# Kernel optimization log

Measured on AMD Instinct MI355X. Metric: run time of the kernel, lower is better.

## Reference

```python
import jax, jax.numpy as jnp
import numpy as np

S = 7          # grid
BBOX = 2       # boxes per cell
C = 20         # classes
IOU_T = 0.5
SCORE_T = 0.05
ORIG_H, ORIG_W = 448.0, 448.0
N = S * S * BBOX  # 98 candidate boxes per image


def _pairwise_iou(b):
    # b: [N,4] xyxy -> [N,N] IoU
    area = jnp.maximum(b[:, 2] - b[:, 0], 0.0) * jnp.maximum(b[:, 3] - b[:, 1], 0.0)
    x1 = jnp.maximum(b[:, None, 0], b[None, :, 0])
    y1 = jnp.maximum(b[:, None, 1], b[None, :, 1])
    x2 = jnp.minimum(b[:, None, 2], b[None, :, 2])
    y2 = jnp.minimum(b[:, None, 3], b[None, :, 3])
    inter = jnp.maximum(x2 - x1, 0.0) * jnp.maximum(y2 - y1, 0.0)
    union = area[:, None] + area[None, :] - inter
    return inter / jnp.maximum(union, 1e-9)


def _nms_keep(boxes, scores):
    # Greedy NMS (same math as torchvision.nms), then score threshold,
    # as in the original (threshold applied AFTER nms). Returns bool keep
    # mask in the ORIGINAL box order.
    order = jnp.argsort(-scores)
    M = _pairwise_iou(boxes[order])
    idx = jnp.arange(N)

    def body(i, keep):
        sup = (M[i] > IOU_T) & (idx > i) & keep[i]
        return keep & ~sup

    keep = jax.lax.fori_loop(0, N, body, jnp.ones(N, dtype=bool))
    keep = keep & (scores[order] >= SCORE_T)
    return jnp.zeros(N, dtype=bool).at[order].set(keep)


def _forward(x):
    B = x.shape[0]
    pred_cls = x[..., :C]                                   # [B,S,S,C]
    off = x[..., C:C + 4 * BBOX].reshape(B, S, S, BBOX, 4)  # [B,S,S,Bbox,4]
    conf = x[..., C + 4 * BBOX:C + 5 * BBOX]                # [B,S,S,Bbox]

    # YOLOv1 decode: cell-relative xy -> normalized image coords; wh already normalized.
    gy, gx = jnp.meshgrid(jnp.arange(S, dtype=x.dtype), jnp.arange(S, dtype=x.dtype), indexing="ij")
    cx = (off[..., 0] + gx[None, :, :, None]) / S
    cy = (off[..., 1] + gy[None, :, :, None]) / S
    w, h = off[..., 2], off[..., 3]
    boxes = jnp.stack([cx - w / 2, cy - h / 2, cx + w / 2, cy + h / 2], axis=-1)
    boxes = jnp.clip(boxes, 0.0, 1.0)
    scale = jnp.array([ORIG_W, ORIG_H, ORIG_W, ORIG_H], dtype=x.dtype)
    boxes_px = (boxes * scale).reshape(B, N, 4)             # [B,N,4] pixel xyxy

    cls_prob = jax.nn.softmax(pred_cls, axis=-1)            # [B,S,S,C]
    scores = (cls_prob[..., None, :] * conf[..., None]).reshape(B, N, C)  # [B,N,C]

    # Per-batch, per-class NMS, fully vectorized (boxes shared across classes).
    keep = jax.vmap(lambda bb, ss: jax.vmap(lambda s: _nms_keep(bb, s))(ss.T))(boxes_px, scores)  # [B,C,N]
    keep = keep.transpose(0, 2, 1).reshape(B, N * C)        # original (S,S,Bbox,C) flatten order

    cls_ids = jnp.tile(jnp.arange(C, dtype=x.dtype), N)     # [N*C]
    boxes_rep = jnp.repeat(boxes_px, C, axis=1)             # [B,N*C,4]
    out = jnp.concatenate([
        jnp.broadcast_to(cls_ids[None, :, None], (B, N * C, 1)),
        boxes_rep,
        scores.reshape(B, N * C, 1),
    ], axis=-1)                                             # [B,N*C,6] = [class,x1,y1,x2,y2,score]
    # Fixed-shape equivalent of the ragged torch output: suppressed rows zeroed.
    return out * keep[..., None].astype(x.dtype)


def setup_inputs() -> dict:
    key = jax.random.key(0)
    return {"inputs_ts": jax.random.normal(key, (1024, S, S, C + 5 * BBOX), dtype=jnp.float32)}


def reference(inputs_ts):
    return _forward(inputs_ts)
```

## Files before the change

### kernel.cpp

```cpp
#include <hip/hip_runtime.h>


namespace {
constexpr int kS    = 7;
constexpr int kC    = 20;
constexpr int kFeat = 30;
constexpr int kN    = 98;
constexpr int kRows = kN * kC;
constexpr int kOutF = kRows * 6;
constexpr int kT    = 256;
constexpr float kIouT   = 0.5f;
constexpr float kScoreT = 0.05f;
}

__device__ __forceinline__ float iou_f(float ax1, float ay1, float ax2, float ay2,
                                       float bx1, float by1, float bx2, float by2) {
#pragma clang fp contract(off)
    float aa = fmaxf(ax2 - ax1, 0.f) * fmaxf(ay2 - ay1, 0.f);
    float ab = fmaxf(bx2 - bx1, 0.f) * fmaxf(by2 - by1, 0.f);
    float ix1 = fmaxf(ax1, bx1);
    float iy1 = fmaxf(ay1, by1);
    float ix2 = fminf(ax2, bx2);
    float iy2 = fminf(ay2, by2);
    float inter = fmaxf(ix2 - ix1, 0.f) * fmaxf(iy2 - iy1, 0.f);
    float uni = aa + ab - inter;
    return inter / fmaxf(uni, 1e-9f);
}

__device__ __forceinline__ unsigned long long shfl64(unsigned long long v, int src) {
    unsigned lo = (unsigned)__shfl((int)(unsigned)(v & 0xffffffffull), src);
    unsigned hi = (unsigned)__shfl((int)(unsigned)(v >> 32), src);
    return ((unsigned long long)hi << 32) | lo;
}

__global__ __launch_bounds__(kT, 4) void yolo_head_kernel(const float* __restrict__ x,
                                                          float* __restrict__ out) {
    __shared__ float xs[kS * kS * kFeat];
    __shared__ float scT[kRows];
    __shared__ float maxp[kS * kS];
    __shared__ float x1s[kN], y1s[kN], x2s[kN], y2s[kN];
    __shared__ unsigned long long adjLo[kN], adjHi[kN];
    __shared__ float csc[4][kN];
    __shared__ unsigned short cid[4][kN];
    __shared__ unsigned short rnk[4][64];
    __shared__ unsigned short rid[4][64];
    __shared__ unsigned km[kC][4];

    const int b   = blockIdx.x;
    const int tid = threadIdx.x;
    const float* xb = x + (size_t)b * (kS * kS * kFeat);

    for (int e = tid; e < (kS * kS * kFeat) / 2; e += kT)
        reinterpret_cast<float2*>(xs)[e] = reinterpret_cast<const float2*>(xb)[e];
    __syncthreads();

    if (tid < kS * kS) {
#pragma clang fp contract(off)
        const int cell = tid;
        const float* p = &xs[cell * kFeat];
        float mx = p[0];
        for (int c = 1; c < kC; ++c) mx = fmaxf(mx, p[c]);
        float e[kC];
        float sum = 0.f;
        for (int c = 0; c < kC; ++c) { e[c] = expf(p[c] - mx); sum += e[c]; }
        const float conf0 = p[28], conf1 = p[29];
        for (int c = 0; c < kC; ++c) {
            float pr = e[c] / sum;
            scT[c * kN + 2 * cell]     = pr * conf0;
            scT[c * kN + 2 * cell + 1] = pr * conf1;
        }
        maxp[cell] = 1.0f / sum;
    } else if (tid >= 64 && tid < 64 + kN) {
#pragma clang fp contract(off)
        const int n = tid - 64;
        const int cell = n >> 1, k = n & 1;
        const int gi = cell / kS, gj = cell % kS;
        const float* p = &xs[cell * kFeat + kC + 4 * k];
        float cx = (p[0] + (float)gj) / 7.0f;
        float cy = (p[1] + (float)gi) / 7.0f;
        float w = p[2], h = p[3];
        x1s[n] = fminf(fmaxf(cx - w * 0.5f, 0.f), 1.f) * 448.f;
        y1s[n] = fminf(fmaxf(cy - h * 0.5f, 0.f), 1.f) * 448.f;
        x2s[n] = fminf(fmaxf(cx + w * 0.5f, 0.f), 1.f) * 448.f;
        y2s[n] = fminf(fmaxf(cy + h * 0.5f, 0.f), 1.f) * 448.f;
    }
    __syncthreads();

    const int wv   = tid >> 6;
    const int lane = tid & 63;
    const int nB   = (lane < kN - 64) ? lane + 64 : 0;

    {
        const float aX1 = x1s[lane], aY1 = y1s[lane], aX2 = x2s[lane], aY2 = y2s[lane];
        const float bX1 = x1s[nB],  bY1 = y1s[nB],  bX2 = x2s[nB],  bY2 = y2s[nB];
        const int cA = lane >> 1, kA = lane & 1;
        const bool uA = xs[cA * kFeat + 28 + kA] * maxp[cA] >= kScoreT;
        bool uB = false;
        if (lane < kN - 64) {
            const int cB = nB >> 1, kB = nB & 1;
            uB = xs[cB * kFeat + 28 + kB] * maxp[cB] >= kScoreT;
        }
        const unsigned long long ULo = __ballot(uA);
        const unsigned long long UHi = __ballot(uB);
        for (int i = wv; i < kN; i += 4) {
            const bool inU = (i < 64) ? ((ULo >> i) & 1ull) : ((UHi >> (i - 64)) & 1ull);
            if (!inU) continue;
            const float iX1 = x1s[i], iY1 = y1s[i], iX2 = x2s[i], iY2 = y2s[i];
            const bool oA = iou_f(iX1, iY1, iX2, iY2, aX1, aY1, aX2, aY2) > kIouT;
            const bool oB = (lane < kN - 64) &&
                            iou_f(iX1, iY1, iX2, iY2, bX1, bY1, bX2, bY2) > kIouT;
            const unsigned long long rLo = __ballot(oA);
            const unsigned long long rHi = __ballot(oB);
            if (lane == 0) { adjLo[i] = rLo; adjHi[i] = rHi; }
        }
    }
    __syncthreads();

    {
        const unsigned long long rowLoA = adjLo[lane], rowHiA = adjHi[lane];
        const unsigned long long rowLoB = adjLo[nB],   rowHiB = adjHi[nB];
        const unsigned long long selfA  = 1ull << lane;
        const unsigned long long lt     = (1ull << lane) - 1ull;
        for (int pass = 0; pass < 5; ++pass) {
            const int c = wv + 4 * pass;

            const float s0 = scT[c * kN + lane];
            const bool  c0 = (s0 >= kScoreT);
            float s1 = 0.f;
            bool  c1 = false;
            if (lane < kN - 64) { s1 = scT[c * kN + 64 + lane]; c1 = (s1 >= kScoreT); }
            const unsigned long long candLo = __ballot(c0);
            const unsigned long long candHi = __ballot(c1);
            const int K = __popcll(candLo) + __popcll(candHi);

            const bool t0 = c0 && ((((rowLoA & candLo) & ~selfA) | (rowHiA & candHi)) != 0ull);
            const bool t1 = c1 && (((rowLoB & candLo) | ((rowHiB & candHi) & ~selfA)) != 0ull);
            const unsigned long long conLo = __ballot(t0);
            const unsigned long long conHi = __ballot(t1);

            unsigned long long keepLo, keepHi;
            if ((conLo | conHi) == 0ull) {
                keepLo = candLo; keepHi = candHi;
            } else if (K <= 64) {
                const int KS0 = __popcll(conLo);
                const int KS  = KS0 + __popcll(conHi);
                int q0 = 0, q1 = 0;
                if (t0) { q0 = __popcll(conLo & lt);       csc[wv][q0] = s0; cid[wv][q0] = (unsigned short)lane; }
                if (t1) { q1 = KS0 + __popcll(conHi & lt); csc[wv][q1] = s1; cid[wv][q1] = (unsigned short)(lane + 64); }
                __builtin_amdgcn_wave_barrier();
                const bool  act = (lane < KS);
                const float sp  = act ? csc[wv][lane] : 0.f;
                int rp = 0;
                for (int q = 0; q < KS; ++q) {
                    const float sq = csc[wv][q];
                    rp += ((sq > sp) || ((sq == sp) && (q < lane))) ? 1 : 0;
                }
                if (act) { rnk[wv][lane] = (unsigned short)rp; rid[wv][rp] = cid[wv][lane]; }
                __builtin_amdgcn_wave_barrier();
                const int myb = act ? (int)rid[wv][lane] : 0;
                const unsigned long long rLo = adjLo[myb];
                const unsigned long long rHi = adjHi[myb];
                unsigned long long supLo = 0, supHi = 0, keepM = 0;
                for (int r = 0; r < KS; ++r) {
                    const int bi = __shfl(myb, r);
                    const unsigned long long qLo = shfl64(rLo, r);
                    const unsigned long long qHi = shfl64(rHi, r);
                    const unsigned long long word = (bi & 64) ? supHi : supLo;
                    const unsigned long long bit  = (word >> (bi & 63)) & 1ull;
                    const unsigned long long take = bit - 1ull;
                    keepM |= (1ull << r) & take;
                    supLo |= qLo & take;
                    supHi |= qHi & take;
                }
                const bool k0 = t0 && ((keepM >> rnk[wv][q0]) & 1ull);
                const bool k1 = t1 && ((keepM >> rnk[wv][q1]) & 1ull);
                keepLo = (candLo & ~conLo) | __ballot(k0);
                keepHi = (candHi & ~conHi) | __ballot(k1);
            } else {
                const int K0 = __popcll(candLo);
                int p0 = 0, p1 = 0;
                if (c0) { p0 = __popcll(candLo & lt);      csc[wv][p0] = s0; cid[wv][p0] = (unsigned short)lane; }
                if (c1) { p1 = K0 + __popcll(candHi & lt); csc[wv][p1] = s1; cid[wv][p1] = (unsigned short)(lane + 64); }
                __builtin_amdgcn_wave_barrier();
                bool al0 = c0, al1 = c1, k0 = false, k1 = false;
                const float n0x1 = x1s[lane], n0y1 = y1s[lane], n0x2 = x2s[lane], n0y2 = y2s[lane];
                const float n1x1 = x1s[nB],  n1y1 = y1s[nB],  n1x2 = x2s[nB],  n1y2 = y2s[nB];
                for (;;) {
                    float bs; int bp;
                    if (al0 && (!al1 || s0 >= s1)) { bs = s0; bp = p0; }
                    else if (al1)                  { bs = s1; bp = p1; }
                    else                           { bs = -1e30f; bp = 1 << 20; }
                    for (int off = 32; off; off >>= 1) {
                        const float os = __shfl_xor(bs, off);
                        const int   op = __shfl_xor(bp, off);
                        if (os > bs || (os == bs && op < bp)) { bs = os; bp = op; }
                    }
                    if (bp >= (1 << 20)) break;
                    const int bi = cid[wv][bp];
                    const float kx1 = x1s[bi], ky1 = y1s[bi], kx2 = x2s[bi], ky2 = y2s[bi];
                    if (bp == p0 && al0) { k0 = true; al0 = false; }
                    if (bp == p1 && al1) { k1 = true; al1 = false; }
                    if (al0 && iou_f(kx1, ky1, kx2, ky2, n0x1, n0y1, n0x2, n0y2) > kIouT) al0 = false;
                    if (al1 && iou_f(kx1, ky1, kx2, ky2, n1x1, n1y1, n1x2, n1y2) > kIouT) al1 = false;
                }
                keepLo = __ballot(k0);
                keepHi = __ballot(k1);
            }
            if (lane == 0) {
                km[c][0] = (unsigned)keepLo;
                km[c][1] = (unsigned)(keepLo >> 32);
                km[c][2] = (unsigned)keepHi;
                km[c][3] = (unsigned)(keepHi >> 32);
            }
        }
    }
    __syncthreads();

    for (int j = tid; j < kRows / 2; j += kT) {
        const int n = j / 10;
        const int c0i = 2 * (j % 10);
        const int c1i = c0i + 1;
        const float sA = scT[c0i * kN + n];
        const float sB = scT[c1i * kN + n];
        const float bbx = x1s[n], bby = y1s[n], bbz = x2s[n], bbw = y2s[n];
        const float mA = ((km[c0i][n >> 5] >> (n & 31)) & 1u) ? 1.f : 0.f;
        const float mB = ((km[c1i][n >> 5] >> (n & 31)) & 1u) ? 1.f : 0.f;
        float* ob = out + (size_t)b * kOutF + (size_t)12 * j;
        float4 q0, q1, q2;
        q0.x = mA * (float)c0i; q0.y = mA * bbx; q0.z = mA * bby; q0.w = mA * bbz;
        q1.x = mA * bbw;        q1.y = mA * sA;  q1.z = mB * (float)c1i; q1.w = mB * bbx;
        q2.x = mB * bby;        q2.y = mB * bbz; q2.z = mB * bbw;        q2.w = mB * sB;
        reinterpret_cast<float4*>(ob)[0] = q0;
        reinterpret_cast<float4*>(ob)[1] = q1;
        reinterpret_cast<float4*>(ob)[2] = q2;
    }
}

extern "C" void kernel_launch(void* const* d_in, const int* in_sizes, int n_in,
                              void* d_out, int out_size, void* d_ws, size_t ws_size,
                              hipStream_t stream) {
    const float* x = (const float*)d_in[0];
    float* out = (float*)d_out;
    const int B = in_sizes[0] / (kS * kS * kFeat);
    hipLaunchKernelGGL(yolo_head_kernel, dim3(B), dim3(kT), 0, stream, x, out);
}
```

Baseline: 83.64 us.

## Use one 64-thread wave per image instead of four waves

Shrinks each block to a single wavefront, so all phases (load, decode, softmax, adjacency build, per-class NMS over all 20 classes, output write) run serially in one wave. Box coordinates are kept in registers, and the adjacency loop walks only set bits of the candidate mask instead of striding over every box. Shared memory per block drops, which lets more blocks fit per CU, and the block barriers become cheap. In exchange, per-block latency grows because the four waves' parallel work, including the 20 classes, is now serialized, and the output stores are issued by fewer threads.

```diff
diff --git a/kernel.cpp b/kernel.cpp
--- a/kernel.cpp
+++ b/kernel.cpp
@@ -8,7 +8,6 @@
 constexpr int kN    = 98;
 constexpr int kRows = kN * kC;
 constexpr int kOutF = kRows * 6;
-constexpr int kT    = 256;
 constexpr float kIouT   = 0.5f;
 constexpr float kScoreT = 0.05f;
 }
@@ -33,66 +32,83 @@
     return ((unsigned long long)hi << 32) | lo;
 }
 
-__global__ __launch_bounds__(kT, 4) void yolo_head_kernel(const float* __restrict__ x,
-                                                          float* __restrict__ out) {
+__global__ __launch_bounds__(64) void yolo_head_kernel(const float* __restrict__ x,
+                                                       float* __restrict__ out) {
     __shared__ float xs[kS * kS * kFeat];
     __shared__ float scT[kRows];
     __shared__ float maxp[kS * kS];
     __shared__ float x1s[kN], y1s[kN], x2s[kN], y2s[kN];
     __shared__ unsigned long long adjLo[kN], adjHi[kN];
-    __shared__ float csc[4][kN];
-    __shared__ unsigned short cid[4][kN];
-    __shared__ unsigned short rnk[4][64];
-    __shared__ unsigned short rid[4][64];
+    __shared__ float csc[kN];
+    __shared__ unsigned short cid[kN];
+    __shared__ unsigned short rnk[64], rid[64];
     __shared__ unsigned km[kC][4];
 
-    const int b   = blockIdx.x;
-    const int tid = threadIdx.x;
+    const int b    = blockIdx.x;
+    const int lane = threadIdx.x;
     const float* xb = x + (size_t)b * (kS * kS * kFeat);
 
-    for (int e = tid; e < (kS * kS * kFeat) / 2; e += kT)
-        reinterpret_cast<float2*>(xs)[e] = reinterpret_cast<const float2*>(xb)[e];
-    __syncthreads();
-
-    if (tid < kS * kS) {
+    {
+        const float2* s = reinterpret_cast<const float2*>(xb);
+        float2* d = reinterpret_cast<float2*>(xs);
+        for (int e = lane; e < (kS * kS * kFeat) / 2; e += 64) d[e] = s[e];
+    }
+    __syncthreads();
+
+    float aX1, aY1, aX2, aY2;
+    float bX1 = 0.f, bY1 = 0.f, bX2 = 0.f, bY2 = 0.f;
+    {
 #pragma clang fp contract(off)
-        const int cell = tid;
-        const float* p = &xs[cell * kFeat];
-        float mx = p[0];
-        for (int c = 1; c < kC; ++c) mx = fmaxf(mx, p[c]);
-        float e[kC];
-        float sum = 0.f;
-        for (int c = 0; c < kC; ++c) { e[c] = expf(p[c] - mx); sum += e[c]; }
-        const float conf0 = p[28], conf1 = p[29];
-        for (int c = 0; c < kC; ++c) {
-            float pr = e[c] / sum;
-            scT[c * kN + 2 * cell]     = pr * conf0;
-            scT[c * kN + 2 * cell + 1] = pr * conf1;
-        }
-        maxp[cell] = 1.0f / sum;
-    } else if (tid >= 64 && tid < 64 + kN) {
-#pragma clang fp contract(off)
-        const int n = tid - 64;
-        const int cell = n >> 1, k = n & 1;
-        const int gi = cell / kS, gj = cell % kS;
-        const float* p = &xs[cell * kFeat + kC + 4 * k];
-        float cx = (p[0] + (float)gj) / 7.0f;
-        float cy = (p[1] + (float)gi) / 7.0f;
-        float w = p[2], h = p[3];
-        x1s[n] = fminf(fmaxf(cx - w * 0.5f, 0.f), 1.f) * 448.f;
-        y1s[n] = fminf(fmaxf(cy - h * 0.5f, 0.f), 1.f) * 448.f;
-        x2s[n] = fminf(fmaxf(cx + w * 0.5f, 0.f), 1.f) * 448.f;
-        y2s[n] = fminf(fmaxf(cy + h * 0.5f, 0.f), 1.f) * 448.f;
-    }
-    __syncthreads();
-
-    const int wv   = tid >> 6;
-    const int lane = tid & 63;
-    const int nB   = (lane < kN - 64) ? lane + 64 : 0;
-
-    {
-        const float aX1 = x1s[lane], aY1 = y1s[lane], aX2 = x2s[lane], aY2 = y2s[lane];
-        const float bX1 = x1s[nB],  bY1 = y1s[nB],  bX2 = x2s[nB],  bY2 = y2s[nB];
+        {
+            const int n = lane;
+            const int cell = n >> 1, k = n & 1;
+            const int gi = cell / kS, gj = cell % kS;
+            const float* p = &xs[cell * kFeat + kC + 4 * k];
+            float cx = (p[0] + (float)gj) / 7.0f;
+            float cy = (p[1] + (float)gi) / 7.0f;
+            float w = p[2], h = p[3];
+            aX1 = fminf(fmaxf(cx - w * 0.5f, 0.f), 1.f) * 448.f;
+            aY1 = fminf(fmaxf(cy - h * 0.5f, 0.f), 1.f) * 448.f;
+            aX2 = fminf(fmaxf(cx + w * 0.5f, 0.f), 1.f) * 448.f;
+            aY2 = fminf(fmaxf(cy + h * 0.5f, 0.f), 1.f) * 448.f;
+            x1s[n] = aX1; y1s[n] = aY1; x2s[n] = aX2; y2s[n] = aY2;
+        }
+        if (lane < kN - 64) {
+            const int n = lane + 64;
+            const int cell = n >> 1, k = n & 1;
+            const int gi = cell / kS, gj = cell % kS;
+            const float* p = &xs[cell * kFeat + kC + 4 * k];
+            float cx = (p[0] + (float)gj) / 7.0f;
+            float cy = (p[1] + (float)gi) / 7.0f;
+            float w = p[2], h = p[3];
+            bX1 = fminf(fmaxf(cx - w * 0.5f, 0.f), 1.f) * 448.f;
+            bY1 = fminf(fmaxf(cy - h * 0.5f, 0.f), 1.f) * 448.f;
+            bX2 = fminf(fmaxf(cx + w * 0.5f, 0.f), 1.f) * 448.f;
+            bY2 = fminf(fmaxf(cy + h * 0.5f, 0.f), 1.f) * 448.f;
+            x1s[n] = bX1; y1s[n] = bY1; x2s[n] = bX2; y2s[n] = bY2;
+        }
+        if (lane < kS * kS) {
+            const int cell = lane;
+            const float* p = &xs[cell * kFeat];
+            float mx = p[0];
+            for (int c = 1; c < kC; ++c) mx = fmaxf(mx, p[c]);
+            float e[kC];
+            float sum = 0.f;
+            for (int c = 0; c < kC; ++c) { e[c] = expf(p[c] - mx); sum += e[c]; }
+            const float conf0 = p[28], conf1 = p[29];
+            for (int c = 0; c < kC; ++c) {
+                float pr = e[c] / sum;
+                scT[c * kN + 2 * cell]     = pr * conf0;
+                scT[c * kN + 2 * cell + 1] = pr * conf1;
+            }
+            maxp[cell] = 1.0f / sum;
+        }
+    }
+    __syncthreads();
+
+    const int nB = (lane < kN - 64) ? lane + 64 : 0;
+
+    {
         const int cA = lane >> 1, kA = lane & 1;
         const bool uA = xs[cA * kFeat + 28 + kA] * maxp[cA] >= kScoreT;
         bool uB = false;
@@ -102,9 +118,10 @@
         }
         const unsigned long long ULo = __ballot(uA);
         const unsigned long long UHi = __ballot(uB);
-        for (int i = wv; i < kN; i += 4) {
-            const bool inU = (i < 64) ? ((ULo >> i) & 1ull) : ((UHi >> (i - 64)) & 1ull);
-            if (!inU) continue;
+        unsigned long long m = ULo;
+        while (m) {
+            const int i = __builtin_ctzll(m);
+            m &= m - 1;
             const float iX1 = x1s[i], iY1 = y1s[i], iX2 = x2s[i], iY2 = y2s[i];
             const bool oA = iou_f(iX1, iY1, iX2, iY2, aX1, aY1, aX2, aY2) > kIouT;
             const bool oB = (lane < kN - 64) &&
@@ -113,6 +130,18 @@
             const unsigned long long rHi = __ballot(oB);
             if (lane == 0) { adjLo[i] = rLo; adjHi[i] = rHi; }
         }
+        m = UHi;
+        while (m) {
+            const int i = 64 + __builtin_ctzll(m);
+            m &= m - 1;
+            const float iX1 = x1s[i], iY1 = y1s[i], iX2 = x2s[i], iY2 = y2s[i];
+            const bool oA = iou_f(iX1, iY1, iX2, iY2, aX1, aY1, aX2, aY2) > kIouT;
+            const bool oB = (lane < kN - 64) &&
+                            iou_f(iX1, iY1, iX2, iY2, bX1, bY1, bX2, bY2) > kIouT;
+            const unsigned long long rLo = __ballot(oA);
+            const unsigned long long rHi = __ballot(oB);
+            if (lane == 0) { adjLo[i] = rLo; adjHi[i] = rHi; }
+        }
     }
     __syncthreads();
 
@@ -121,9 +150,7 @@
         const unsigned long long rowLoB = adjLo[nB],   rowHiB = adjHi[nB];
         const unsigned long long selfA  = 1ull << lane;
         const unsigned long long lt     = (1ull << lane) - 1ull;
-        for (int pass = 0; pass < 5; ++pass) {
-            const int c = wv + 4 * pass;
-
+        for (int c = 0; c < kC; ++c) {
             const float s0 = scT[c * kN + lane];
             const bool  c0 = (s0 >= kScoreT);
             float s1 = 0.f;
@@ -145,19 +172,19 @@
                 const int KS0 = __popcll(conLo);
                 const int KS  = KS0 + __popcll(conHi);
                 int q0 = 0, q1 = 0;
-                if (t0) { q0 = __popcll(conLo & lt);       csc[wv][q0] = s0; cid[wv][q0] = (unsigned short)lane; }
-                if (t1) { q1 = KS0 + __popcll(conHi & lt); csc[wv][q1] = s1; cid[wv][q1] = (unsigned short)(lane + 64); }
+                if (t0) { q0 = __popcll(conLo & lt);       csc[q0] = s0; cid[q0] = (unsigned short)lane; }
+                if (t1) { q1 = KS0 + __popcll(conHi & lt); csc[q1] = s1; cid[q1] = (unsigned short)(lane + 64); }
                 __builtin_amdgcn_wave_barrier();
                 const bool  act = (lane < KS);
-                const float sp  = act ? csc[wv][lane] : 0.f;
+                const float sp  = act ? csc[lane] : 0.f;
                 int rp = 0;
                 for (int q = 0; q < KS; ++q) {
-                    const float sq = csc[wv][q];
+                    const float sq = csc[q];
                     rp += ((sq > sp) || ((sq == sp) && (q < lane))) ? 1 : 0;
                 }
-                if (act) { rnk[wv][lane] = (unsigned short)rp; rid[wv][rp] = cid[wv][lane]; }
+                if (act) { rnk[lane] = (unsigned short)rp; rid[rp] = cid[lane]; }
                 __builtin_amdgcn_wave_barrier();
-                const int myb = act ? (int)rid[wv][lane] : 0;
+                const int myb = act ? (int)rid[lane] : 0;
                 const unsigned long long rLo = adjLo[myb];
                 const unsigned long long rHi = adjHi[myb];
                 unsigned long long supLo = 0, supHi = 0, keepM = 0;
@@ -172,19 +199,17 @@
                     supLo |= qLo & take;
                     supHi |= qHi & take;
                 }
-                const bool k0 = t0 && ((keepM >> rnk[wv][q0]) & 1ull);
-                const bool k1 = t1 && ((keepM >> rnk[wv][q1]) & 1ull);
+                const bool k0 = t0 && ((keepM >> rnk[q0]) & 1ull);
+                const bool k1 = t1 && ((keepM >> rnk[q1]) & 1ull);
                 keepLo = (candLo & ~conLo) | __ballot(k0);
                 keepHi = (candHi & ~conHi) | __ballot(k1);
             } else {
                 const int K0 = __popcll(candLo);
                 int p0 = 0, p1 = 0;
-                if (c0) { p0 = __popcll(candLo & lt);      csc[wv][p0] = s0; cid[wv][p0] = (unsigned short)lane; }
-                if (c1) { p1 = K0 + __popcll(candHi & lt); csc[wv][p1] = s1; cid[wv][p1] = (unsigned short)(lane + 64); }
+                if (c0) { p0 = __popcll(candLo & lt);      csc[p0] = s0; cid[p0] = (unsigned short)lane; }
+                if (c1) { p1 = K0 + __popcll(candHi & lt); csc[p1] = s1; cid[p1] = (unsigned short)(lane + 64); }
                 __builtin_amdgcn_wave_barrier();
                 bool al0 = c0, al1 = c1, k0 = false, k1 = false;
-                const float n0x1 = x1s[lane], n0y1 = y1s[lane], n0x2 = x2s[lane], n0y2 = y2s[lane];
-                const float n1x1 = x1s[nB],  n1y1 = y1s[nB],  n1x2 = x2s[nB],  n1y2 = y2s[nB];
                 for (;;) {
                     float bs; int bp;
                     if (al0 && (!al1 || s0 >= s1)) { bs = s0; bp = p0; }
@@ -196,12 +221,12 @@
                         if (os > bs || (os == bs && op < bp)) { bs = os; bp = op; }
                     }
                     if (bp >= (1 << 20)) break;
-                    const int bi = cid[wv][bp];
+                    const int bi = cid[bp];
                     const float kx1 = x1s[bi], ky1 = y1s[bi], kx2 = x2s[bi], ky2 = y2s[bi];
                     if (bp == p0 && al0) { k0 = true; al0 = false; }
                     if (bp == p1 && al1) { k1 = true; al1 = false; }
-                    if (al0 && iou_f(kx1, ky1, kx2, ky2, n0x1, n0y1, n0x2, n0y2) > kIouT) al0 = false;
-                    if (al1 && iou_f(kx1, ky1, kx2, ky2, n1x1, n1y1, n1x2, n1y2) > kIouT) al1 = false;
+                    if (al0 && iou_f(kx1, ky1, kx2, ky2, aX1, aY1, aX2, aY2) > kIouT) al0 = false;
+                    if (al1 && iou_f(kx1, ky1, kx2, ky2, bX1, bY1, bX2, bY2) > kIouT) al1 = false;
                 }
                 keepLo = __ballot(k0);
                 keepHi = __ballot(k1);
@@ -216,7 +241,7 @@
     }
     __syncthreads();
 
-    for (int j = tid; j < kRows / 2; j += kT) {
+    for (int j = lane; j < kRows / 2; j += 64) {
         const int n = j / 10;
         const int c0i = 2 * (j % 10);
         const int c1i = c0i + 1;
@@ -242,5 +267,5 @@
     const float* x = (const float*)d_in[0];
     float* out = (float*)d_out;
     const int B = in_sizes[0] / (kS * kS * kFeat);
-    hipLaunchKernelGGL(yolo_head_kernel, dim3(B), dim3(kT), 0, stream, x, out);
-}
+    hipLaunchKernelGGL(yolo_head_kernel, dim3(B), dim3(64), 0, stream, x, out);
+}
```

Result: slower. 122.4 us (+46.4%).

## Split each image's 20 classes across two blocks to double grid parallelism

Applied to the files above, without the earlier changes.

Launches two blocks per image, each handling 10 of the 20 classes for NMS scoring and output writing. This halves the per-block score buffer and class-loop length, and the launch bound is raised so more blocks can be resident. In exchange, both blocks redundantly load the input, compute the softmax, decode boxes and build the IoU adjacency matrix. Waves 0-1 now handle three classes and waves 2-3 two, which leaves the waves unevenly loaded.

```diff
diff --git a/kernel.cpp b/kernel.cpp
--- a/kernel.cpp
+++ b/kernel.cpp
@@ -6,6 +6,7 @@
 constexpr int kC    = 20;
 constexpr int kFeat = 30;
 constexpr int kN    = 98;
+constexpr int kHC   = 10;
 constexpr int kRows = kN * kC;
 constexpr int kOutF = kRows * 6;
 constexpr int kT    = 256;
@@ -33,10 +34,10 @@
     return ((unsigned long long)hi << 32) | lo;
 }
 
-__global__ __launch_bounds__(kT, 4) void yolo_head_kernel(const float* __restrict__ x,
+__global__ __launch_bounds__(kT, 8) void yolo_head_kernel(const float* __restrict__ x,
                                                           float* __restrict__ out) {
     __shared__ float xs[kS * kS * kFeat];
-    __shared__ float scT[kRows];
+    __shared__ float scTh[kHC * kN];
     __shared__ float maxp[kS * kS];
     __shared__ float x1s[kN], y1s[kN], x2s[kN], y2s[kN];
     __shared__ unsigned long long adjLo[kN], adjHi[kN];
@@ -44,9 +45,10 @@
     __shared__ unsigned short cid[4][kN];
     __shared__ unsigned short rnk[4][64];
     __shared__ unsigned short rid[4][64];
-    __shared__ unsigned km[kC][4];
-
-    const int b   = blockIdx.x;
+    __shared__ unsigned km[kHC][4];
+
+    const int b   = blockIdx.x >> 1;
+    const int h   = blockIdx.x & 1;
     const int tid = threadIdx.x;
     const float* xb = x + (size_t)b * (kS * kS * kFeat);
 
@@ -64,10 +66,11 @@
         float sum = 0.f;
         for (int c = 0; c < kC; ++c) { e[c] = expf(p[c] - mx); sum += e[c]; }
         const float conf0 = p[28], conf1 = p[29];
-        for (int c = 0; c < kC; ++c) {
+        for (int lc = 0; lc < kHC; ++lc) {
+            const int c = kHC * h + lc;
             float pr = e[c] / sum;
-            scT[c * kN + 2 * cell]     = pr * conf0;
-            scT[c * kN + 2 * cell + 1] = pr * conf1;
+            scTh[lc * kN + 2 * cell]     = pr * conf0;
+            scTh[lc * kN + 2 * cell + 1] = pr * conf1;
         }
         maxp[cell] = 1.0f / sum;
     } else if (tid >= 64 && tid < 64 + kN) {
@@ -78,11 +81,11 @@
         const float* p = &xs[cell * kFeat + kC + 4 * k];
         float cx = (p[0] + (float)gj) / 7.0f;
         float cy = (p[1] + (float)gi) / 7.0f;
-        float w = p[2], h = p[3];
+        float w = p[2], h2 = p[3];
         x1s[n] = fminf(fmaxf(cx - w * 0.5f, 0.f), 1.f) * 448.f;
-        y1s[n] = fminf(fmaxf(cy - h * 0.5f, 0.f), 1.f) * 448.f;
+        y1s[n] = fminf(fmaxf(cy - h2 * 0.5f, 0.f), 1.f) * 448.f;
         x2s[n] = fminf(fmaxf(cx + w * 0.5f, 0.f), 1.f) * 448.f;
-        y2s[n] = fminf(fmaxf(cy + h * 0.5f, 0.f), 1.f) * 448.f;
+        y2s[n] = fminf(fmaxf(cy + h2 * 0.5f, 0.f), 1.f) * 448.f;
     }
     __syncthreads();
 
@@ -121,14 +124,19 @@
         const unsigned long long rowLoB = adjLo[nB],   rowHiB = adjHi[nB];
         const unsigned long long selfA  = 1ull << lane;
         const unsigned long long lt     = (1ull << lane) - 1ull;
-        for (int pass = 0; pass < 5; ++pass) {
-            const int c = wv + 4 * pass;
-
-            const float s0 = scT[c * kN + lane];
+        const int ncl = (wv < 2) ? 3 : 2;
+        float ps0[3], ps1[3];
+        for (int k = 0; k < ncl; ++k) {
+            const int lc = wv + 4 * k;
+            ps0[k] = scTh[lc * kN + lane];
+            ps1[k] = (lane < kN - 64) ? scTh[lc * kN + 64 + lane] : 0.f;
+        }
+        for (int k = 0; k < ncl; ++k) {
+            const int lc = wv + 4 * k;
+            const float s0 = ps0[k];
+            const float s1 = ps1[k];
             const bool  c0 = (s0 >= kScoreT);
-            float s1 = 0.f;
-            bool  c1 = false;
-            if (lane < kN - 64) { s1 = scT[c * kN + 64 + lane]; c1 = (s1 >= kScoreT); }
+            const bool  c1 = (lane < kN - 64) && (s1 >= kScoreT);
             const unsigned long long candLo = __ballot(c0);
             const unsigned long long candHi = __ballot(c1);
             const int K = __popcll(candLo) + __popcll(candHi);
@@ -207,25 +215,27 @@
                 keepHi = __ballot(k1);
             }
             if (lane == 0) {
-                km[c][0] = (unsigned)keepLo;
-                km[c][1] = (unsigned)(keepLo >> 32);
-                km[c][2] = (unsigned)keepHi;
-                km[c][3] = (unsigned)(keepHi >> 32);
+                km[lc][0] = (unsigned)keepLo;
+                km[lc][1] = (unsigned)(keepLo >> 32);
+                km[lc][2] = (unsigned)keepHi;
+                km[lc][3] = (unsigned)(keepHi >> 32);
             }
         }
     }
     __syncthreads();
 
-    for (int j = tid; j < kRows / 2; j += kT) {
-        const int n = j / 10;
-        const int c0i = 2 * (j % 10);
+    for (int t = tid; t < (kRows / 2) / 2; t += kT) {
+        const int n   = t / 5;
+        const int q   = 5 * h + t % 5;
+        const int lc0 = 2 * (t % 5);
+        const int c0i = kHC * h + lc0;
         const int c1i = c0i + 1;
-        const float sA = scT[c0i * kN + n];
-        const float sB = scT[c1i * kN + n];
+        const float sA = scTh[lc0 * kN + n];
+        const float sB = scTh[(lc0 + 1) * kN + n];
         const float bbx = x1s[n], bby = y1s[n], bbz = x2s[n], bbw = y2s[n];
-        const float mA = ((km[c0i][n >> 5] >> (n & 31)) & 1u) ? 1.f : 0.f;
-        const float mB = ((km[c1i][n >> 5] >> (n & 31)) & 1u) ? 1.f : 0.f;
-        float* ob = out + (size_t)b * kOutF + (size_t)12 * j;
+        const float mA = ((km[lc0][n >> 5] >> (n & 31)) & 1u) ? 1.f : 0.f;
+        const float mB = ((km[lc0 + 1][n >> 5] >> (n & 31)) & 1u) ? 1.f : 0.f;
+        float* ob = out + (size_t)b * kOutF + (size_t)12 * (n * 10 + q);
         float4 q0, q1, q2;
         q0.x = mA * (float)c0i; q0.y = mA * bbx; q0.z = mA * bby; q0.w = mA * bbz;
         q1.x = mA * bbw;        q1.y = mA * sA;  q1.z = mB * (float)c1i; q1.w = mB * bbx;
@@ -242,5 +252,5 @@
     const float* x = (const float*)d_in[0];
     float* out = (float*)d_out;
     const int B = in_sizes[0] / (kS * kS * kFeat);
-    hipLaunchKernelGGL(yolo_head_kernel, dim3(B), dim3(kT), 0, stream, x, out);
-}
+    hipLaunchKernelGGL(yolo_head_kernel, dim3(2 * B), dim3(kT), 0, stream, x, out);
+}
```

Measured after the change: 102.9 us. +23.0%, slower.

## Write output rows directly from NMS passes and replace IoU division with compare

Applied to the files above, without the earlier changes.

The separate output phase, its keep-mask shared array and the final block barrier are removed. Each wave now writes its class's output rows directly, as strided float2 stores, as soon as that class's NMS finishes. The IoU threshold test drops the float division and instead compares inter against union times a double-precision constant to keep the rounding behaviour. The rank array is replaced by a ballot, and box coordinates are hoisted into registers. Risks are less coalesced strided stores (each lane writes 24-byte pieces 480 bytes apart) and added cost from the double-precision compare.

```diff
diff --git a/kernel.cpp b/kernel.cpp
--- a/kernel.cpp
+++ b/kernel.cpp
@@ -9,11 +9,11 @@
 constexpr int kRows = kN * kC;
 constexpr int kOutF = kRows * 6;
 constexpr int kT    = 256;
-constexpr float kIouT   = 0.5f;
 constexpr float kScoreT = 0.05f;
-}
-
-__device__ __forceinline__ float iou_f(float ax1, float ay1, float ax2, float ay2,
+constexpr double kIouCmp = 0.50000001490116119384765625;
+}
+
+__device__ __forceinline__ bool iou_gt(float ax1, float ay1, float ax2, float ay2,
                                        float bx1, float by1, float bx2, float by2) {
 #pragma clang fp contract(off)
     float aa = fmaxf(ax2 - ax1, 0.f) * fmaxf(ay2 - ay1, 0.f);
@@ -23,8 +23,8 @@
     float ix2 = fminf(ax2, bx2);
     float iy2 = fminf(ay2, by2);
     float inter = fmaxf(ix2 - ix1, 0.f) * fmaxf(iy2 - iy1, 0.f);
-    float uni = aa + ab - inter;
-    return inter / fmaxf(uni, 1e-9f);
+    float udiv = fmaxf(aa + ab - inter, 1e-9f);
+    return (double)inter > (double)udiv * kIouCmp;
 }
 
 __device__ __forceinline__ unsigned long long shfl64(unsigned long long v, int src) {
@@ -42,9 +42,7 @@
     __shared__ unsigned long long adjLo[kN], adjHi[kN];
     __shared__ float csc[4][kN];
     __shared__ unsigned short cid[4][kN];
-    __shared__ unsigned short rnk[4][64];
     __shared__ unsigned short rid[4][64];
-    __shared__ unsigned km[kC][4];
 
     const int b   = blockIdx.x;
     const int tid = threadIdx.x;
@@ -78,25 +76,27 @@
         const float* p = &xs[cell * kFeat + kC + 4 * k];
         float cx = (p[0] + (float)gj) / 7.0f;
         float cy = (p[1] + (float)gi) / 7.0f;
-        float w = p[2], h = p[3];
+        float w = p[2], h2 = p[3];
         x1s[n] = fminf(fmaxf(cx - w * 0.5f, 0.f), 1.f) * 448.f;
-        y1s[n] = fminf(fmaxf(cy - h * 0.5f, 0.f), 1.f) * 448.f;
+        y1s[n] = fminf(fmaxf(cy - h2 * 0.5f, 0.f), 1.f) * 448.f;
         x2s[n] = fminf(fmaxf(cx + w * 0.5f, 0.f), 1.f) * 448.f;
-        y2s[n] = fminf(fmaxf(cy + h * 0.5f, 0.f), 1.f) * 448.f;
+        y2s[n] = fminf(fmaxf(cy + h2 * 0.5f, 0.f), 1.f) * 448.f;
     }
     __syncthreads();
 
     const int wv   = tid >> 6;
     const int lane = tid & 63;
-    const int nB   = (lane < kN - 64) ? lane + 64 : 0;
+    const bool hasB = (lane < kN - 64);
+    const int nB   = hasB ? lane + 64 : 0;
+
+    const float aX1 = x1s[lane], aY1 = y1s[lane], aX2 = x2s[lane], aY2 = y2s[lane];
+    const float bX1 = x1s[nB],  bY1 = y1s[nB],  bX2 = x2s[nB],  bY2 = y2s[nB];
 
     {
-        const float aX1 = x1s[lane], aY1 = y1s[lane], aX2 = x2s[lane], aY2 = y2s[lane];
-        const float bX1 = x1s[nB],  bY1 = y1s[nB],  bX2 = x2s[nB],  bY2 = y2s[nB];
         const int cA = lane >> 1, kA = lane & 1;
         const bool uA = xs[cA * kFeat + 28 + kA] * maxp[cA] >= kScoreT;
         bool uB = false;
-        if (lane < kN - 64) {
+        if (hasB) {
             const int cB = nB >> 1, kB = nB & 1;
             uB = xs[cB * kFeat + 28 + kB] * maxp[cB] >= kScoreT;
         }
@@ -106,9 +106,8 @@
             const bool inU = (i < 64) ? ((ULo >> i) & 1ull) : ((UHi >> (i - 64)) & 1ull);
             if (!inU) continue;
             const float iX1 = x1s[i], iY1 = y1s[i], iX2 = x2s[i], iY2 = y2s[i];
-            const bool oA = iou_f(iX1, iY1, iX2, iY2, aX1, aY1, aX2, aY2) > kIouT;
-            const bool oB = (lane < kN - 64) &&
-                            iou_f(iX1, iY1, iX2, iY2, bX1, bY1, bX2, bY2) > kIouT;
+            const bool oA = iou_gt(iX1, iY1, iX2, iY2, aX1, aY1, aX2, aY2);
+            const bool oB = hasB && iou_gt(iX1, iY1, iX2, iY2, bX1, bY1, bX2, bY2);
             const unsigned long long rLo = __ballot(oA);
             const unsigned long long rHi = __ballot(oB);
             if (lane == 0) { adjLo[i] = rLo; adjHi[i] = rHi; }
@@ -121,14 +120,16 @@
         const unsigned long long rowLoB = adjLo[nB],   rowHiB = adjHi[nB];
         const unsigned long long selfA  = 1ull << lane;
         const unsigned long long lt     = (1ull << lane) - 1ull;
+        float* const obA = out + (size_t)b * kOutF + (size_t)lane * (kC * 6);
+        float* const obB = obA + 64 * (kC * 6);
+
         for (int pass = 0; pass < 5; ++pass) {
             const int c = wv + 4 * pass;
 
             const float s0 = scT[c * kN + lane];
+            const float s1 = hasB ? scT[c * kN + 64 + lane] : 0.f;
             const bool  c0 = (s0 >= kScoreT);
-            float s1 = 0.f;
-            bool  c1 = false;
-            if (lane < kN - 64) { s1 = scT[c * kN + 64 + lane]; c1 = (s1 >= kScoreT); }
+            const bool  c1 = hasB && (s1 >= kScoreT);
             const unsigned long long candLo = __ballot(c0);
             const unsigned long long candHi = __ballot(c1);
             const int K = __popcll(candLo) + __popcll(candHi);
@@ -138,9 +139,9 @@
             const unsigned long long conLo = __ballot(t0);
             const unsigned long long conHi = __ballot(t1);
 
-            unsigned long long keepLo, keepHi;
+            bool k0, k1;
             if ((conLo | conHi) == 0ull) {
-                keepLo = candLo; keepHi = candHi;
+                k0 = c0; k1 = c1;
             } else if (K <= 64) {
                 const int KS0 = __popcll(conLo);
                 const int KS  = KS0 + __popcll(conHi);
@@ -155,7 +156,7 @@
                     const float sq = csc[wv][q];
                     rp += ((sq > sp) || ((sq == sp) && (q < lane))) ? 1 : 0;
                 }
-                if (act) { rnk[wv][lane] = (unsigned short)rp; rid[wv][rp] = cid[wv][lane]; }
+                if (act) rid[wv][rp] = cid[wv][lane];
                 __builtin_amdgcn_wave_barrier();
                 const int myb = act ? (int)rid[wv][lane] : 0;
                 const unsigned long long rLo = adjLo[myb];
@@ -172,19 +173,17 @@
                     supLo |= qLo & take;
                     supHi |= qHi & take;
                 }
-                const bool k0 = t0 && ((keepM >> rnk[wv][q0]) & 1ull);
-                const bool k1 = t1 && ((keepM >> rnk[wv][q1]) & 1ull);
-                keepLo = (candLo & ~conLo) | __ballot(k0);
-                keepHi = (candHi & ~conHi) | __ballot(k1);
+                const unsigned long long posKeep = __ballot(act && ((keepM >> rp) & 1ull));
+                k0 = c0 && (!t0 || ((posKeep >> q0) & 1ull));
+                k1 = c1 && (!t1 || ((posKeep >> q1) & 1ull));
             } else {
                 const int K0 = __popcll(candLo);
                 int p0 = 0, p1 = 0;
                 if (c0) { p0 = __popcll(candLo & lt);      csc[wv][p0] = s0; cid[wv][p0] = (unsigned short)lane; }
                 if (c1) { p1 = K0 + __popcll(candHi & lt); csc[wv][p1] = s1; cid[wv][p1] = (unsigned short)(lane + 64); }
                 __builtin_amdgcn_wave_barrier();
-                bool al0 = c0, al1 = c1, k0 = false, k1 = false;
-                const float n0x1 = x1s[lane], n0y1 = y1s[lane], n0x2 = x2s[lane], n0y2 = y2s[lane];
-                const float n1x1 = x1s[nB],  n1y1 = y1s[nB],  n1x2 = x2s[nB],  n1y2 = y2s[nB];
+                bool al0 = c0, al1 = c1;
+                k0 = false; k1 = false;
                 for (;;) {
                     float bs; int bp;
                     if (al0 && (!al1 || s0 >= s1)) { bs = s0; bp = p0; }
@@ -200,39 +199,26 @@
                     const float kx1 = x1s[bi], ky1 = y1s[bi], kx2 = x2s[bi], ky2 = y2s[bi];
                     if (bp == p0 && al0) { k0 = true; al0 = false; }
                     if (bp == p1 && al1) { k1 = true; al1 = false; }
-                    if (al0 && iou_f(kx1, ky1, kx2, ky2, n0x1, n0y1, n0x2, n0y2) > kIouT) al0 = false;
-                    if (al1 && iou_f(kx1, ky1, kx2, ky2, n1x1, n1y1, n1x2, n1y2) > kIouT) al1 = false;
-                }
-                keepLo = __ballot(k0);
-                keepHi = __ballot(k1);
+                    if (al0 && iou_gt(kx1, ky1, kx2, ky2, aX1, aY1, aX2, aY2)) al0 = false;
+                    if (al1 && iou_gt(kx1, ky1, kx2, ky2, bX1, bY1, bX2, bY2)) al1 = false;
+                }
             }
-            if (lane == 0) {
-                km[c][0] = (unsigned)keepLo;
-                km[c][1] = (unsigned)(keepLo >> 32);
-                km[c][2] = (unsigned)keepHi;
-                km[c][3] = (unsigned)(keepHi >> 32);
+
+            {
+                const float mA = k0 ? 1.f : 0.f;
+                float2* rA = reinterpret_cast<float2*>(obA + c * 6);
+                rA[0] = make_float2(mA * (float)c, mA * aX1);
+                rA[1] = make_float2(mA * aY1,      mA * aX2);
+                rA[2] = make_float2(mA * aY2,      mA * s0);
+                if (hasB) {
+                    const float mB = k1 ? 1.f : 0.f;
+                    float2* rB = reinterpret_cast<float2*>(obB + c * 6);
+                    rB[0] = make_float2(mB * (float)c, mB * bX1);
+                    rB[1] = make_float2(mB * bY1,      mB * bX2);
+                    rB[2] = make_float2(mB * bY2,      mB * s1);
+                }
             }
         }
-    }
-    __syncthreads();
-
-    for (int j = tid; j < kRows / 2; j += kT) {
-        const int n = j / 10;
-        const int c0i = 2 * (j % 10);
-        const int c1i = c0i + 1;
-        const float sA = scT[c0i * kN + n];
-        const float sB = scT[c1i * kN + n];
-        const float bbx = x1s[n], bby = y1s[n], bbz = x2s[n], bbw = y2s[n];
-        const float mA = ((km[c0i][n >> 5] >> (n & 31)) & 1u) ? 1.f : 0.f;
-        const float mB = ((km[c1i][n >> 5] >> (n & 31)) & 1u) ? 1.f : 0.f;
-        float* ob = out + (size_t)b * kOutF + (size_t)12 * j;
-        float4 q0, q1, q2;
-        q0.x = mA * (float)c0i; q0.y = mA * bbx; q0.z = mA * bby; q0.w = mA * bbz;
-        q1.x = mA * bbw;        q1.y = mA * sA;  q1.z = mB * (float)c1i; q1.w = mB * bbx;
-        q2.x = mB * bby;        q2.y = mB * bbz; q2.z = mB * bbw;        q2.w = mB * sB;
-        reinterpret_cast<float4*>(ob)[0] = q0;
-        reinterpret_cast<float4*>(ob)[1] = q1;
-        reinterpret_cast<float4*>(ob)[2] = q2;
     }
 }
 
```

Result: slower. 90.00 us (+7.6%).
